# Performance work log

Hardware: AMD Instinct MI355X
Metric: run time of the kernel (lower is better)

Reference implementation:

```python
import jax, jax.numpy as jnp
import numpy as np

R_BLOCKS = 8  # r: number of diagonal blocks

def _rotate(Wp, R):
    # Wp: [out, in], R: [r, b, b] with in = r*b.
    # Equivalent to Wp @ block_diag(R[0],...,R[r-1]) without materializing [in,in].
    o = Wp.shape[0]
    r, b, _ = R.shape
    Wb = Wp.reshape(o, r, b)
    return jnp.einsum('ori,rij->orj', Wb, R).reshape(o, r * b)

def setup_inputs() -> dict:
    key = jax.random.key(0)
    ks = jax.random.split(key, 6)
    in_f, out_f, r = 1024, 1024, R_BLOCKS
    blk = in_f // r
    return {
        'attn': jax.random.normal(ks[0], (3 * out_f, in_f), jnp.float32) * 0.02,
        'bias': jax.random.normal(ks[1], (3 * out_f,), jnp.float32) * 0.02,
        'x': jax.random.normal(ks[2], (4, 2048, in_f), jnp.float32),
        'q_R': jax.random.normal(ks[3], (r, blk, blk), jnp.float32) * 0.02,
        'k_R': jax.random.normal(ks[4], (r, blk, blk), jnp.float32) * 0.02,
        'v_R': jax.random.normal(ks[5], (r, blk, blk), jnp.float32) * 0.02,
    }

def reference(attn, bias, x, q_R, k_R, v_R):
    # attn.data in torch detaches the frozen pretrained weight
    W = jax.lax.stop_gradient(attn)
    Wq, Wk, Wv = jnp.split(W, 3, axis=0)
    filt = jnp.concatenate([_rotate(Wq, q_R), _rotate(Wk, k_R), _rotate(Wv, v_R)], axis=0)
    # F.linear: x @ filt.T + bias -> [B, S, 3*out]
    return jnp.einsum('bsi,oi->bso', x, filt) + bias
```

## Files before the change

### kernel.cpp

```cpp
#include <hip/hip_runtime.h>
#include <hip/hip_bf16.h>
#include <stdint.h>

typedef __attribute__((ext_vector_type(8))) short short8;
typedef __attribute__((ext_vector_type(4))) float floatx4;

#define M_TOT 8192
#define N_TOT 3072
#define K_TOT 1024
#define BM 128
#define BN 128
#define BK 64

__device__ inline unsigned short f2bf(float f) {
    union { float f; unsigned int ui; } v; v.f = f;
    unsigned int x = v.ui;
    unsigned int r = (x + 0x7fffu + ((x >> 16) & 1u)) >> 16;
    return (unsigned short)r;
}

__device__ inline void gl2lds16(const void* g, void* l) {
    __builtin_amdgcn_global_load_lds(
        (__attribute__((address_space(1))) void*)g,
        (__attribute__((address_space(3))) void*)l,
        16, 0, 0);
}

__global__ __launch_bounds__(256) void cvt_f32_bf16_kernel(
    const float* __restrict__ in, unsigned short* __restrict__ out, int n8)
{
    int i = blockIdx.x * 256 + threadIdx.x;
    if (i >= n8) return;
    const float4* p = (const float4*)in + (size_t)i * 2;
    float4 a = p[0], b = p[1];
    short8 s;
    s[0] = (short)f2bf(a.x); s[1] = (short)f2bf(a.y);
    s[2] = (short)f2bf(a.z); s[3] = (short)f2bf(a.w);
    s[4] = (short)f2bf(b.x); s[5] = (short)f2bf(b.y);
    s[6] = (short)f2bf(b.z); s[7] = (short)f2bf(b.w);
    *(short8*)(out + (size_t)i * 8) = s;
}

__global__ __launch_bounds__(256) void rotate_w_kernel(
    const float* __restrict__ W,
    const float* __restrict__ qR,
    const float* __restrict__ kR,
    const float* __restrict__ vR,
    unsigned short* __restrict__ Fout)
{
    __shared__ float Rs[128 * 128];
    __shared__ float Ws[64 * 128];

    const int tid = threadIdx.x;
    const int o0 = blockIdx.x * 64;
    const int r = blockIdx.y;

    const float* R = (o0 < 1024) ? qR : (o0 < 2048) ? kR : vR;
    R += (size_t)r * 128 * 128;

#pragma unroll
    for (int i = 0; i < 16; ++i) {
        int idx = (i * 256 + tid) * 4;
        *(float4*)(Rs + idx) = *(const float4*)(R + idx);
    }
#pragma unroll
    for (int i = 0; i < 8; ++i) {
        int idx = (i * 256 + tid) * 4;
        int row = idx >> 7;
        int col = idx & 127;
        *(float4*)(Ws + idx) =
            *(const float4*)(W + (size_t)(o0 + row) * K_TOT + r * 128 + col);
    }
    __syncthreads();

    const int jg = (tid & 15) * 8;
    const int ob = tid >> 4;

    float acc[4][8];
#pragma unroll
    for (int a = 0; a < 4; ++a)
#pragma unroll
        for (int b = 0; b < 8; ++b) acc[a][b] = 0.f;

    for (int i = 0; i < 128; ++i) {
        float4 r0 = *(const float4*)(Rs + i * 128 + jg);
        float4 r1 = *(const float4*)(Rs + i * 128 + jg + 4);
        float rv[8] = {r0.x, r0.y, r0.z, r0.w, r1.x, r1.y, r1.z, r1.w};
#pragma unroll
        for (int oo = 0; oo < 4; ++oo) {
            float wv = Ws[(ob + oo * 16) * 128 + i];
#pragma unroll
            for (int t = 0; t < 8; ++t) acc[oo][t] += wv * rv[t];
        }
    }

#pragma unroll
    for (int oo = 0; oo < 4; ++oo) {
        int o = o0 + ob + oo * 16;
        short8 s;
#pragma unroll
        for (int t = 0; t < 8; ++t) s[t] = (short)f2bf(acc[oo][t]);
        *(short8*)(Fout + (size_t)o * K_TOT + r * 128 + jg) = s;
    }
}

__global__ void gemm_bt_kernel(
    const unsigned short* __restrict__ X,
    const unsigned short* __restrict__ F,
    const float* __restrict__ bias,
    float* __restrict__ out)
{
    __shared__ unsigned short As[BM * BK];
    __shared__ unsigned short Bs[BN * BK];

    const int tid = threadIdx.x;
    const int wave = tid >> 6;
    const int lane = tid & 63;
    const int m0 = blockIdx.x * BM;
    const int n0 = blockIdx.y * BN;

    const int wm = wave >> 1;
    const int wn = wave & 1;
    const int quad = lane >> 4;
    const int l15 = lane & 15;

    const int srow_lane = lane >> 3;
    const int scol = (lane & 7) * 8;

    floatx4 acc[4][4];
#pragma unroll
    for (int a = 0; a < 4; ++a)
#pragma unroll
        for (int b = 0; b < 4; ++b) acc[a][b] = (floatx4){0.f, 0.f, 0.f, 0.f};

    for (int k0 = 0; k0 < K_TOT; k0 += BK) {
#pragma unroll
        for (int p = 0; p < 4; ++p) {
            const int rr = (wave * 4 + p) * 8 + srow_lane;
            gl2lds16(X + (size_t)(m0 + rr) * K_TOT + k0 + scol,
                     As + (wave * 4 + p) * 512 + lane * 8);
            gl2lds16(F + (size_t)(n0 + rr) * K_TOT + k0 + scol,
                     Bs + (wave * 4 + p) * 512 + lane * 8);
        }
        __syncthreads();

#pragma unroll
        for (int ks = 0; ks < 2; ++ks) {
            short8 a[4], b[4];
#pragma unroll
            for (int mi = 0; mi < 4; ++mi)
                a[mi] = *(const short8*)(As + (wm * 64 + mi * 16 + l15) * BK +
                                         ks * 32 + quad * 8);
#pragma unroll
            for (int ni = 0; ni < 4; ++ni)
                b[ni] = *(const short8*)(Bs + (wn * 64 + ni * 16 + l15) * BK +
                                         ks * 32 + quad * 8);
#pragma unroll
            for (int mi = 0; mi < 4; ++mi)
#pragma unroll
                for (int ni = 0; ni < 4; ++ni)
                    acc[mi][ni] = __builtin_amdgcn_mfma_f32_16x16x32_bf16(
                        a[mi], b[ni], acc[mi][ni], 0, 0, 0);
        }
        __syncthreads();
    }

#pragma unroll
    for (int ni = 0; ni < 4; ++ni) {
        const int col = n0 + wn * 64 + ni * 16 + l15;
        const float bv = bias[col];
#pragma unroll
        for (int mi = 0; mi < 4; ++mi) {
            const int rbase = m0 + wm * 64 + mi * 16 + quad * 4;
#pragma unroll
            for (int reg = 0; reg < 4; ++reg) {
                out[(size_t)(rbase + reg) * N_TOT + col] =
                    acc[mi][ni][reg] + bv;
            }
        }
    }
}

extern "C" void kernel_launch(void* const* d_in, const int* in_sizes, int n_in,
                              void* d_out, int out_size, void* d_ws, size_t ws_size,
                              hipStream_t stream) {
    const float* attn = (const float*)d_in[0];
    const float* bias = (const float*)d_in[1];
    const float* x    = (const float*)d_in[2];
    const float* qR   = (const float*)d_in[3];
    const float* kR   = (const float*)d_in[4];
    const float* vR   = (const float*)d_in[5];

    float* out = (float*)d_out;

    unsigned short* xb   = (unsigned short*)d_ws;
    unsigned short* filt = xb + (size_t)M_TOT * K_TOT;

    const int n8 = (M_TOT * K_TOT) / 8;
    cvt_f32_bf16_kernel<<<n8 / 256, 256, 0, stream>>>(x, xb, n8);
    rotate_w_kernel<<<dim3(48, 8), 256, 0, stream>>>(attn, qR, kR, vR, filt);
    gemm_bt_kernel<<<dim3(M_TOT / BM, N_TOT / BN), 256, 0, stream>>>(
        xb, filt, bias, out);
}
```

Before: 217.1 us.

## Swizzle GEMM LDS tiles and stage epilogue through LDS for coalesced stores

XOR-swizzles the 16-byte column groups of the A/B shared-memory tiles on both the global-to-LDS write side and the MFMA fragment read side, to cut LDS bank conflicts. It also reuses the shared buffer to stage the output tile in two halves, so each thread writes float4 rows to global memory instead of scattered scalar stores. The cost is extra barriers and LDS traffic in the epilogue.

After: 215.5 us. Within noise of the previous version (-0.7%).

```diff
diff --git a/kernel.cpp b/kernel.cpp
--- a/kernel.cpp
+++ b/kernel.cpp
@@ -110,8 +110,10 @@
     const float* __restrict__ bias,
     float* __restrict__ out)
 {
-    __shared__ unsigned short As[BM * BK];
-    __shared__ unsigned short Bs[BN * BK];
+    __shared__ __align__(16) unsigned char smem[2 * BM * BK * sizeof(unsigned short)];
+    unsigned short* As = (unsigned short*)smem;
+    unsigned short* Bs = As + BM * BK;
+    float* Cs = (float*)smem;
 
     const int tid = threadIdx.x;
     const int wave = tid >> 6;
@@ -125,7 +127,8 @@
     const int l15 = lane & 15;
 
     const int srow_lane = lane >> 3;
-    const int scol = (lane & 7) * 8;
+    const int scg = (lane & 7) ^ srow_lane;
+    const int scol = scg * 8;
 
     floatx4 acc[4][4];
 #pragma unroll
@@ -146,15 +149,14 @@
 
 #pragma unroll
         for (int ks = 0; ks < 2; ++ks) {
+            const int fcg = ((ks * 4 + quad) ^ (l15 & 7)) * 8;
             short8 a[4], b[4];
 #pragma unroll
             for (int mi = 0; mi < 4; ++mi)
-                a[mi] = *(const short8*)(As + (wm * 64 + mi * 16 + l15) * BK +
-                                         ks * 32 + quad * 8);
+                a[mi] = *(const short8*)(As + (wm * 64 + mi * 16 + l15) * BK + fcg);
 #pragma unroll
             for (int ni = 0; ni < 4; ++ni)
-                b[ni] = *(const short8*)(Bs + (wn * 64 + ni * 16 + l15) * BK +
-                                         ks * 32 + quad * 8);
+                b[ni] = *(const short8*)(Bs + (wn * 64 + ni * 16 + l15) * BK + fcg);
 #pragma unroll
             for (int mi = 0; mi < 4; ++mi)
 #pragma unroll
@@ -165,19 +167,36 @@
         __syncthreads();
     }
 
-#pragma unroll
-    for (int ni = 0; ni < 4; ++ni) {
-        const int col = n0 + wn * 64 + ni * 16 + l15;
-        const float bv = bias[col];
-#pragma unroll
-        for (int mi = 0; mi < 4; ++mi) {
-            const int rbase = m0 + wm * 64 + mi * 16 + quad * 4;
-#pragma unroll
-            for (int reg = 0; reg < 4; ++reg) {
-                out[(size_t)(rbase + reg) * N_TOT + col] =
-                    acc[mi][ni][reg] + bv;
-            }
-        }
+    float bv[4];
+#pragma unroll
+    for (int ni = 0; ni < 4; ++ni)
+        bv[ni] = bias[n0 + wn * 64 + ni * 16 + l15];
+
+#pragma unroll
+    for (int h = 0; h < 2; ++h) {
+        if (wm == h) {
+#pragma unroll
+            for (int mi = 0; mi < 4; ++mi)
+#pragma unroll
+                for (int ni = 0; ni < 4; ++ni) {
+                    const int col = wn * 64 + ni * 16 + l15;
+#pragma unroll
+                    for (int reg = 0; reg < 4; ++reg) {
+                        const int row = mi * 16 + quad * 4 + reg;
+                        Cs[row * 128 + col] = acc[mi][ni][reg] + bv[ni];
+                    }
+                }
+        }
+        __syncthreads();
+#pragma unroll
+        for (int t = 0; t < 8; ++t) {
+            const int idx = t * 256 + tid;
+            const int row = idx >> 5;
+            const int c4 = (idx & 31) * 4;
+            float4 v = *(const float4*)(Cs + row * 128 + c4);
+            *(float4*)(out + (size_t)(m0 + h * 64 + row) * N_TOT + n0 + c4) = v;
+        }
+        __syncthreads();
     }
 }
 
```
